# Performance work log

Hardware: AMD Instinct MI355X
Metric: run time of the kernel (lower is better)

The kernel has to match this reference:

```python
import jax, jax.numpy as jnp
import numpy as np

LN2 = float(np.log(2.0))
N_ATOMS = 100_000
N_PAIRS = 2_000_000
F = 64     # number_of_atom_features
R = 16     # number_of_radial_basis_functions
N_RES = 3


def setup_inputs() -> dict:
    key = jax.random.key(0)
    ks = jax.random.split(key, 16)
    s = 0.05
    inp = {
        "pair_indices": jax.random.randint(ks[0], (2, N_PAIRS), 0, N_ATOMS, dtype=jnp.int32),
        "f_ij": jax.random.normal(ks[1], (N_PAIRS, 1, R), dtype=jnp.float32),
        "d_ij": jax.random.uniform(ks[2], (N_PAIRS, 1), dtype=jnp.float32),
        "atomic_embedding": jax.random.normal(ks[3], (N_ATOMS, F), dtype=jnp.float32),
        # AttentionMask parameter G: [F, R]
        "G": jax.random.normal(ks[4], (F, R), dtype=jnp.float32),
        # interaction_i / interaction_j linear layers (stored as [in, out])
        "Wi": jax.random.normal(ks[5], (F, F), dtype=jnp.float32) * s,
        "bi": jnp.zeros((F,), dtype=jnp.float32),
        "Wj": jax.random.normal(ks[6], (F, F), dtype=jnp.float32) * s,
        "bj": jnp.zeros((F,), dtype=jnp.float32),
        # residual blocks, stacked over N_RES
        "res_W1": jax.random.normal(ks[7], (N_RES, F, F), dtype=jnp.float32) * s,
        "res_b1": jnp.zeros((N_RES, F), dtype=jnp.float32),
        "res_W2": jax.random.normal(ks[8], (N_RES, F, F), dtype=jnp.float32) * s,
        "res_b2": jnp.zeros((N_RES, F), dtype=jnp.float32),
        # process_v linear
        "Wv": jax.random.normal(ks[9], (F, F), dtype=jnp.float32) * s,
        "bv": jnp.zeros((F,), dtype=jnp.float32),
    }
    return inp


def reference(pair_indices, f_ij, d_ij, atomic_embedding,
              G, Wi, bi, Wj, bj, res_W1, res_b1, res_W2, res_b2, Wv, bv):
    idx_i, idx_j = pair_indices[0], pair_indices[1]
    f = f_ij.squeeze(1)                                  # [P, R]

    # ShiftedSoftplus on node embeddings
    x = jax.nn.softplus(atomic_embedding) - LN2          # [N, F]

    x_i_prime = jax.nn.softplus(x @ Wi + bi)             # [N, F]
    x_j_prime = jax.nn.softplus(x[idx_j] @ Wj + bj)      # [P, F] (gather)
    f_prime = f @ G.T                                    # [P, F] attention mask

    msg = x_j_prime * f_prime                            # [P, F]
    summed = jax.ops.segment_sum(msg, idx_i, num_segments=atomic_embedding.shape[0])

    v = x_i_prime + summed                               # [N, F]
    for l in range(res_W1.shape[0]):
        h = jax.nn.softplus(v @ res_W1[l] + res_b1[l])
        v = v + (h @ res_W2[l] + res_b2[l])
    return jax.nn.softplus(v) @ Wv + bv
```

## Files before the change

### kernel.cpp

```cpp
#include <hip/hip_runtime.h>
#include <math.h>

#define FDIM 64
#define RDIM 16
#define LN2F 0.69314718055994530942f
#define LTS 68
#define NBINR 14336
#define NCHUNK 64

typedef __bf16 bf8_t __attribute__((ext_vector_type(8)));
typedef float  f4_t  __attribute__((ext_vector_type(4)));
typedef _Float16 h2_t __attribute__((ext_vector_type(2)));

__device__ __forceinline__ float sp(float x) {
    return fmaxf(x, 0.0f) + __logf(1.0f + __expf(-fabsf(x)));
}

__device__ __forceinline__ float fdot2f(h2_t a, h2_t b, float c) {
#if __has_builtin(__builtin_amdgcn_fdot2)
    return __builtin_amdgcn_fdot2(a, b, c, false);
#else
    return c + (float)a[0] * (float)b[0] + (float)a[1] * (float)b[1];
#endif
}

__device__ __forceinline__ void cvt_store16(_Float16* dst, float4 A, float4 B,
                                            float4 C4, float4 D)
{
    h2_t hv[8];
    hv[0] = h2_t{(_Float16)A.x,  (_Float16)A.y};
    hv[1] = h2_t{(_Float16)A.z,  (_Float16)A.w};
    hv[2] = h2_t{(_Float16)B.x,  (_Float16)B.y};
    hv[3] = h2_t{(_Float16)B.z,  (_Float16)B.w};
    hv[4] = h2_t{(_Float16)C4.x, (_Float16)C4.y};
    hv[5] = h2_t{(_Float16)C4.z, (_Float16)C4.w};
    hv[6] = h2_t{(_Float16)D.x,  (_Float16)D.y};
    hv[7] = h2_t{(_Float16)D.z,  (_Float16)D.w};
    *(uint4*)dst       = *(const uint4*)&hv[0];
    *(uint4*)(dst + 8) = *(const uint4*)&hv[4];
}

__global__ __launch_bounds__(256) void k_prep(
    const float* s0, const float* s1, const float* s2, const float* s3,
    const float* s4, const float* s5, const float* s6, const float* s7,
    const float* s8, __bf16* __restrict__ dst)
{
    const float* srcs[9] = {s0, s1, s2, s3, s4, s5, s6, s7, s8};
    const float* W = srcs[blockIdx.x];
    __bf16* d = dst + (size_t)blockIdx.x * 4096;
    for (int slot = threadIdx.x; slot < 512; slot += 256) {
        int f = slot >> 6, l = slot & 63;
        int kt = f >> 2, nt = f & 3;
        int row0 = kt * 32 + (l >> 4) * 8;
        int col = nt * 16 + (l & 15);
#pragma unroll
        for (int j = 0; j < 8; ++j)
            d[slot * 8 + j] = (__bf16)W[(row0 + j) * FDIM + col];
    }
}

__global__ __launch_bounds__(256) void k_hist2(
    const int* __restrict__ idx_i, int* __restrict__ Cmat,
    int P, int N, int nRange)
{
    __shared__ int h[NBINR];
    const int chunk = blockIdx.x / nRange;
    const int range = blockIdx.x % nRange;
    const int lo = range * NBINR;
    const int nb = min(NBINR, N - lo);
    for (int u = threadIdx.x; u < NBINR; u += 256) h[u] = 0;
    __syncthreads();

    const int chunkSz = (P + NCHUNK - 1) / NCHUNK;
    const int cs = chunk * chunkSz;
    const int ce = min(P, cs + chunkSz);
    int p = cs + threadIdx.x;
    for (; p + 768 < ce; p += 1024) {
        int i0 = idx_i[p];
        int i1 = idx_i[p + 256];
        int i2 = idx_i[p + 512];
        int i3 = idx_i[p + 768];
        unsigned u0 = (unsigned)(i0 - lo);
        unsigned u1 = (unsigned)(i1 - lo);
        unsigned u2 = (unsigned)(i2 - lo);
        unsigned u3 = (unsigned)(i3 - lo);
        if (u0 < (unsigned)nb) atomicAdd(&h[u0], 1);
        if (u1 < (unsigned)nb) atomicAdd(&h[u1], 1);
        if (u2 < (unsigned)nb) atomicAdd(&h[u2], 1);
        if (u3 < (unsigned)nb) atomicAdd(&h[u3], 1);
    }
    for (; p < ce; p += 256) {
        unsigned u = (unsigned)(idx_i[p] - lo);
        if (u < (unsigned)nb) atomicAdd(&h[u], 1);
    }
    __syncthreads();
    for (int u = threadIdx.x; u < nb; u += 256)
        Cmat[(size_t)chunk * N + lo + u] = h[u];
}

__global__ __launch_bounds__(256) void k_scanR(
    int* __restrict__ Cmat, int* __restrict__ tot, int N)
{
    const int bA = blockIdx.x * 512 + threadIdx.x;
    const int bB = bA + 256;
    const bool okA = bA < N, okB = bB < N;
    int runA = 0, runB = 0;
    for (int c = 0; c < NCHUNK; ++c) {
        const size_t base = (size_t)c * N;
        if (okA) { int val = Cmat[base + bA]; Cmat[base + bA] = runA; runA += val; }
        if (okB) { int val = Cmat[base + bB]; Cmat[base + bB] = runB; runB += val; }
    }
    if (okA) tot[bA] = runA;
    if (okB) tot[bB] = runB;
}

__device__ __forceinline__ void tile_in(float* T, const float* __restrict__ src,
                                        int a0, int rows, int lane)
{
#pragma unroll 4
    for (int i = 0; i < 16; ++i) {
        int r = i * 4 + (lane >> 4);
        int col = (lane & 15) * 4;
        float4 val = make_float4(0.f, 0.f, 0.f, 0.f);
        if (r < rows) val = *(const float4*)&src[(size_t)(a0 + r) * FDIM + col];
        *(float4*)&T[r * LTS + col] = val;
    }
}

__device__ __forceinline__ void build_a(const float* T, int lane, bool actLn2,
                                        bf8_t (&aF)[4][2])
{
    const int l15 = lane & 15, quad = lane >> 4;
#pragma unroll
    for (int mt = 0; mt < 4; ++mt) {
#pragma unroll
        for (int kt = 0; kt < 2; ++kt) {
            const float* rp = &T[(mt * 16 + l15) * LTS + kt * 32 + quad * 8];
            float4 u0 = *(const float4*)rp;
            float4 u1 = *(const float4*)(rp + 4);
            float e[8] = {u0.x, u0.y, u0.z, u0.w, u1.x, u1.y, u1.z, u1.w};
            bf8_t f;
#pragma unroll
            for (int j = 0; j < 8; ++j) {
                float t = actLn2 ? (sp(e[j]) - LN2F) : e[j];
                f[j] = (__bf16)t;
            }
            aF[mt][kt] = f;
        }
    }
}

__global__ __launch_bounds__(256) void k_atoms(
    const float* __restrict__ emb, const __bf16* __restrict__ wf,
    const float* __restrict__ bi, const float* __restrict__ bj,
    float* __restrict__ v, float* __restrict__ y, int N)
{
    __shared__ float tile[4][64 * LTS];
    const int lane = threadIdx.x & 63;
    const int wv = threadIdx.x >> 6;
    float* T = tile[wv];
    const int l15 = lane & 15, quad = lane >> 4;

    const bf8_t* wiF = (const bf8_t*)wf;
    const bf8_t* wjF = (const bf8_t*)(wf + 4096);
    bf8_t wi[2][4], wj[2][4];
#pragma unroll
    for (int kt = 0; kt < 2; ++kt)
#pragma unroll
        for (int nt = 0; nt < 4; ++nt) {
            wi[kt][nt] = wiF[(kt * 4 + nt) * 64 + lane];
            wj[kt][nt] = wjF[(kt * 4 + nt) * 64 + lane];
        }
    float biv[4], bjv[4];
#pragma unroll
    for (int nt = 0; nt < 4; ++nt) {
        biv[nt] = bi[nt * 16 + l15];
        bjv[nt] = bj[nt * 16 + l15];
    }

    const int nTiles = (N + 63) >> 6;
    for (int t = blockIdx.x * 4 + wv; t < nTiles; t += gridDim.x * 4) {
        const int a0 = t << 6;
        const int rows = min(64, N - a0);
        tile_in(T, emb, a0, rows, lane);
        bf8_t aF[4][2];
        build_a(T, lane, true, aF);
#pragma unroll
        for (int mt = 0; mt < 4; ++mt)
#pragma unroll
            for (int nt = 0; nt < 4; ++nt) {
                f4_t acc = {biv[nt], biv[nt], biv[nt], biv[nt]};
                acc = __builtin_amdgcn_mfma_f32_16x16x32_bf16(aF[mt][0], wi[0][nt], acc, 0, 0, 0);
                acc = __builtin_amdgcn_mfma_f32_16x16x32_bf16(aF[mt][1], wi[1][nt], acc, 0, 0, 0);
#pragma unroll
                for (int reg = 0; reg < 4; ++reg) {
                    int r = mt * 16 + quad * 4 + reg;
                    if (r < rows) v[(size_t)(a0 + r) * FDIM + nt * 16 + l15] = sp(acc[reg]);
                }
            }
#pragma unroll
        for (int mt = 0; mt < 4; ++mt)
#pragma unroll
            for (int nt = 0; nt < 4; ++nt) {
                f4_t acc = {bjv[nt], bjv[nt], bjv[nt], bjv[nt]};
                acc = __builtin_amdgcn_mfma_f32_16x16x32_bf16(aF[mt][0], wj[0][nt], acc, 0, 0, 0);
                acc = __builtin_amdgcn_mfma_f32_16x16x32_bf16(aF[mt][1], wj[1][nt], acc, 0, 0, 0);
#pragma unroll
                for (int reg = 0; reg < 4; ++reg) {
                    int r = mt * 16 + quad * 4 + reg;
                    if (r < rows) y[(size_t)(a0 + r) * FDIM + nt * 16 + l15] = sp(acc[reg]);
                }
            }
    }
}

__global__ __launch_bounds__(256) void k_post(
    const __bf16* __restrict__ wf,
    const float* __restrict__ rb1, const float* __restrict__ rb2,
    const float* __restrict__ bv,
    float* __restrict__ v, int N)
{
    __shared__ float tile[4][64 * LTS];
    const int lane = threadIdx.x & 63;
    const int wv = threadIdx.x >> 6;
    float* T = tile[wv];
    const int l15 = lane & 15, quad = lane >> 4;

    float b1v[3][4], b2v[3][4], bvv[4];
#pragma unroll
    for (int l = 0; l < 3; ++l)
#pragma unroll
        for (int nt = 0; nt < 4; ++nt) {
            b1v[l][nt] = rb1[l * FDIM + nt * 16 + l15];
            b2v[l][nt] = rb2[l * FDIM + nt * 16 + l15];
        }
#pragma unroll
    for (int nt = 0; nt < 4; ++nt) bvv[nt] = bv[nt * 16 + l15];

    const int nTiles = (N + 63) >> 6;
    for (int t = blockIdx.x * 4 + wv; t < nTiles; t += gridDim.x * 4) {
        const int a0 = t << 6;
        const int rows = min(64, N - a0);
        tile_in(T, v, a0, rows, lane);
        float vC[16][4];
#pragma unroll
        for (int mt = 0; mt < 4; ++mt)
#pragma unroll
            for (int nt = 0; nt < 4; ++nt)
#pragma unroll
                for (int reg = 0; reg < 4; ++reg)
                    vC[mt * 4 + nt][reg] =
                        T[(mt * 16 + quad * 4 + reg) * LTS + nt * 16 + l15];

        for (int l = 0; l < 3; ++l) {
            const bf8_t* w1f = (const bf8_t*)(wf + (size_t)(2 * l) * 4096);
            const bf8_t* w2f = (const bf8_t*)(wf + (size_t)(2 * l + 1) * 4096);
            bf8_t aF[4][2];
            build_a(T, lane, false, aF);
#pragma unroll
            for (int mt = 0; mt < 4; ++mt)
#pragma unroll
                for (int nt = 0; nt < 4; ++nt) {
                    f4_t acc = {b1v[l][nt], b1v[l][nt], b1v[l][nt], b1v[l][nt]};
                    acc = __builtin_amdgcn_mfma_f32_16x16x32_bf16(aF[mt][0], w1f[(0 * 4 + nt) * 64 + lane], acc, 0, 0, 0);
                    acc = __builtin_amdgcn_mfma_f32_16x16x32_bf16(aF[mt][1], w1f[(1 * 4 + nt) * 64 + lane], acc, 0, 0, 0);
#pragma unroll
                    for (int reg = 0; reg < 4; ++reg)
                        T[(mt * 16 + quad * 4 + reg) * LTS + nt * 16 + l15] = sp(acc[reg]);
                }
            bf8_t hF[4][2];
            build_a(T, lane, false, hF);
#pragma unroll
            for (int mt = 0; mt < 4; ++mt)
#pragma unroll
                for (int nt = 0; nt < 4; ++nt) {
                    f4_t acc = {b2v[l][nt], b2v[l][nt], b2v[l][nt], b2v[l][nt]};
                    acc = __builtin_amdgcn_mfma_f32_16x16x32_bf16(hF[mt][0], w2f[(0 * 4 + nt) * 64 + lane], acc, 0, 0, 0);
                    acc = __builtin_amdgcn_mfma_f32_16x16x32_bf16(hF[mt][1], w2f[(1 * 4 + nt) * 64 + lane], acc, 0, 0, 0);
#pragma unroll
                    for (int reg = 0; reg < 4; ++reg)
                        vC[mt * 4 + nt][reg] += acc[reg];
                }
            if (l < 2) {
#pragma unroll
                for (int mt = 0; mt < 4; ++mt)
#pragma unroll
                    for (int nt = 0; nt < 4; ++nt)
#pragma unroll
                        for (int reg = 0; reg < 4; ++reg)
                            T[(mt * 16 + quad * 4 + reg) * LTS + nt * 16 + l15] =
                                vC[mt * 4 + nt][reg];
            }
        }
#pragma unroll
        for (int mt = 0; mt < 4; ++mt)
#pragma unroll
            for (int nt = 0; nt < 4; ++nt)
#pragma unroll
                for (int reg = 0; reg < 4; ++reg)
                    T[(mt * 16 + quad * 4 + reg) * LTS + nt * 16 + l15] =
                        sp(vC[mt * 4 + nt][reg]);
        bf8_t fF[4][2];
        build_a(T, lane, false, fF);
        const bf8_t* wvf = (const bf8_t*)(wf + (size_t)6 * 4096);
#pragma unroll
        for (int mt = 0; mt < 4; ++mt)
#pragma unroll
            for (int nt = 0; nt < 4; ++nt) {
                f4_t acc = {bvv[nt], bvv[nt], bvv[nt], bvv[nt]};
                acc = __builtin_amdgcn_mfma_f32_16x16x32_bf16(fF[mt][0], wvf[(0 * 4 + nt) * 64 + lane], acc, 0, 0, 0);
                acc = __builtin_amdgcn_mfma_f32_16x16x32_bf16(fF[mt][1], wvf[(1 * 4 + nt) * 64 + lane], acc, 0, 0, 0);
#pragma unroll
                for (int reg = 0; reg < 4; ++reg) {
                    int r = mt * 16 + quad * 4 + reg;
                    if (r < rows) v[(size_t)(a0 + r) * FDIM + nt * 16 + l15] = acc[reg];
                }
            }
    }
}

__global__ __launch_bounds__(256) void k_scan_a(
    const int* __restrict__ cnt, int* __restrict__ part, int N)
{
    __shared__ int red[256];
    int b = blockIdx.x, t = threadIdx.x;
    int base = b * 1024 + t * 4;
    int s = 0;
#pragma unroll
    for (int i = 0; i < 4; ++i) { int a = base + i; if (a < N) s += cnt[a]; }
    red[t] = s; __syncthreads();
    for (int off = 128; off > 0; off >>= 1) {
        if (t < off) red[t] += red[t + off];
        __syncthreads();
    }
    if (t == 0) part[b] = red[0];
}

__global__ __launch_bounds__(256) void k_scan_b(int* __restrict__ part, int nPart)
{
    __shared__ int lds[256];
    int t = threadIdx.x;
    int base = t * 4;
    int v[4]; int s = 0;
#pragma unroll
    for (int i = 0; i < 4; ++i) { v[i] = (base + i < nPart) ? part[base + i] : 0; s += v[i]; }
    lds[t] = s; __syncthreads();
    int run = s;
    for (int off = 1; off < 256; off <<= 1) {
        int x = (t >= off) ? lds[t - off] : 0;
        __syncthreads();
        lds[t] += x;
        __syncthreads();
    }
    int excl = lds[t] - run;
#pragma unroll
    for (int i = 0; i < 4; ++i) { if (base + i < nPart) { part[base + i] = excl; excl += v[i]; } }
}

__global__ __launch_bounds__(256) void k_scan_c(
    const int* __restrict__ cnt, const int* __restrict__ part,
    int* __restrict__ start, int N, int P)
{
    __shared__ int lds[256];
    int b = blockIdx.x, t = threadIdx.x;
    int base = b * 1024 + t * 4;
    int v[4]; int s = 0;
#pragma unroll
    for (int i = 0; i < 4; ++i) { int a = base + i; v[i] = (a < N) ? cnt[a] : 0; s += v[i]; }
    lds[t] = s; __syncthreads();
    int run = s;
    for (int off = 1; off < 256; off <<= 1) {
        int x = (t >= off) ? lds[t - off] : 0;
        __syncthreads();
        lds[t] += x;
        __syncthreads();
    }
    int pre = part[b] + (lds[t] - run);
#pragma unroll
    for (int i = 0; i < 4; ++i) {
        int a = base + i;
        if (a < N) { start[a] = pre; pre += v[i]; }
    }
    if (b == 0 && t == 0) start[N] = P;
}

__global__ __launch_bounds__(256) void k_scatter2(
    const int* __restrict__ pidx, const int* __restrict__ Cmat,
    const int* __restrict__ start, int2* __restrict__ sorted,
    int P, int N, int nRange)
{
    __shared__ int cur[NBINR];
    const int chunk = blockIdx.x / nRange;
    const int range = blockIdx.x % nRange;
    const int lo = range * NBINR;
    const int nb = min(NBINR, N - lo);
    for (int u = threadIdx.x; u < nb; u += 256)
        cur[u] = start[lo + u] + Cmat[(size_t)chunk * N + lo + u];
    __syncthreads();

    const int chunkSz = (P + NCHUNK - 1) / NCHUNK;
    const int cs = chunk * chunkSz;
    const int ce = min(P, cs + chunkSz);
    int p = cs + threadIdx.x;
    for (; p + 768 < ce; p += 1024) {
        int i0 = pidx[p];
        int i1 = pidx[p + 256];
        int i2 = pidx[p + 512];
        int i3 = pidx[p + 768];
        int j0 = pidx[P + p];
        int j1 = pidx[P + p + 256];
        int j2 = pidx[P + p + 512];
        int j3 = pidx[P + p + 768];
        unsigned u0 = (unsigned)(i0 - lo);
        unsigned u1 = (unsigned)(i1 - lo);
        unsigned u2 = (unsigned)(i2 - lo);
        unsigned u3 = (unsigned)(i3 - lo);
        if (u0 < (unsigned)nb) { int pos = atomicAdd(&cur[u0], 1); sorted[pos] = make_int2(p, j0); }
        if (u1 < (unsigned)nb) { int pos = atomicAdd(&cur[u1], 1); sorted[pos] = make_int2(p + 256, j1); }
        if (u2 < (unsigned)nb) { int pos = atomicAdd(&cur[u2], 1); sorted[pos] = make_int2(p + 512, j2); }
        if (u3 < (unsigned)nb) { int pos = atomicAdd(&cur[u3], 1); sorted[pos] = make_int2(p + 768, j3); }
    }
    for (; p < ce; p += 256) {
        int i = pidx[p];
        unsigned u = (unsigned)(i - lo);
        if (u < (unsigned)nb) {
            int j = pidx[P + p];
            int pos = atomicAdd(&cur[u], 1);
            sorted[pos] = make_int2(p, j);
        }
    }
}

__global__ __launch_bounds__(256) void k_gatherF(
    const int2* __restrict__ sorted, const float* __restrict__ f_ij,
    int* __restrict__ sortedJ, _Float16* __restrict__ sortedF, int P)
{
    int t = blockIdx.x * blockDim.x + threadIdx.x;
    int n = gridDim.x * blockDim.x;
    int pos = t;
    for (; pos + 3 * n < P; pos += 4 * n) {
        int2 E0 = sorted[pos];
        int2 E1 = sorted[pos + n];
        int2 E2 = sorted[pos + 2 * n];
        int2 E3 = sorted[pos + 3 * n];
        const float4* f0 = (const float4*)(f_ij + (size_t)E0.x * RDIM);
        const float4* f1 = (const float4*)(f_ij + (size_t)E1.x * RDIM);
        const float4* f2 = (const float4*)(f_ij + (size_t)E2.x * RDIM);
        const float4* f3 = (const float4*)(f_ij + (size_t)E3.x * RDIM);
        float4 a0 = f0[0], b0 = f0[1], c0 = f0[2], d0 = f0[3];
        float4 a1 = f1[0], b1 = f1[1], c1 = f1[2], d1 = f1[3];
        float4 a2 = f2[0], b2 = f2[1], c2 = f2[2], d2 = f2[3];
        float4 a3 = f3[0], b3 = f3[1], c3 = f3[2], d3 = f3[3];
        sortedJ[pos]         = E0.y;
        sortedJ[pos + n]     = E1.y;
        sortedJ[pos + 2 * n] = E2.y;
        sortedJ[pos + 3 * n] = E3.y;
        cvt_store16(sortedF + (size_t)pos * 16,           a0, b0, c0, d0);
        cvt_store16(sortedF + (size_t)(pos + n) * 16,     a1, b1, c1, d1);
        cvt_store16(sortedF + (size_t)(pos + 2 * n) * 16, a2, b2, c2, d2);
        cvt_store16(sortedF + (size_t)(pos + 3 * n) * 16, a3, b3, c3, d3);
    }
    for (; pos < P; pos += n) {
        int2 E = sorted[pos];
        const float4* fp = (const float4*)(f_ij + (size_t)E.x * RDIM);
        float4 A = fp[0], B = fp[1], C4 = fp[2], D = fp[3];
        sortedJ[pos] = E.y;
        cvt_store16(sortedF + (size_t)pos * 16, A, B, C4, D);
    }
}

__global__ __launch_bounds__(256) void k_seg(
    const int* __restrict__ sortedJ, const _Float16* __restrict__ sortedF,
    const int* __restrict__ start, const float* __restrict__ G,
    const float* __restrict__ y, float* __restrict__ v, int N)
{
    const int c = threadIdx.x & 63;
    const int w = __builtin_amdgcn_readfirstlane((blockIdx.x << 2) | (threadIdx.x >> 6));
    const int nw = gridDim.x << 2;

    h2_t g2[8];
    {
        const float4* gp = (const float4*)(G + c * RDIM);
        float4 g0 = gp[0], g1 = gp[1], g2v = gp[2], g3 = gp[3];
        g2[0] = h2_t{(_Float16)g0.x, (_Float16)g0.y};
        g2[1] = h2_t{(_Float16)g0.z, (_Float16)g0.w};
        g2[2] = h2_t{(_Float16)g1.x, (_Float16)g1.y};
        g2[3] = h2_t{(_Float16)g1.z, (_Float16)g1.w};
        g2[4] = h2_t{(_Float16)g2v.x, (_Float16)g2v.y};
        g2[5] = h2_t{(_Float16)g2v.z, (_Float16)g2v.w};
        g2[6] = h2_t{(_Float16)g3.x, (_Float16)g3.y};
        g2[7] = h2_t{(_Float16)g3.z, (_Float16)g3.w};
    }

    for (int a = w; a < N; a += nw) {
        const int s = __builtin_amdgcn_readfirstlane(start[a]);
        const int e = __builtin_amdgcn_readfirstlane(start[a + 1]);
        float vold = v[(size_t)a * FDIM + c];
        float acc0 = 0.f, acc1 = 0.f, acc2 = 0.f, acc3 = 0.f;

        for (int base = s; base < e; base += 64) {
            const int nn = (e - base < 64) ? (e - base) : 64;
            const int li = (c < nn) ? c : (nn - 1);
            const int jkv = sortedJ[base + li];

            int k = 0;
            for (; k + 8 <= nn; k += 8) {
                int jj[8];
#pragma unroll
                for (int u = 0; u < 8; ++u)
                    jj[u] = __builtin_amdgcn_readlane(jkv, k + u);
                float yv[8];
#pragma unroll
                for (int u = 0; u < 8; ++u)
                    yv[u] = y[(size_t)jj[u] * FDIM + c];
                const h2_t* f2 = (const h2_t*)(sortedF + (size_t)(base + k) * 16);
#pragma unroll
                for (int u = 0; u < 8; ++u) {
                    float d = 0.f;
#pragma unroll
                    for (int r = 0; r < 8; ++r)
                        d = fdot2f(f2[u * 8 + r], g2[r], d);
                    if ((u & 3) == 0) acc0 = fmaf(d, yv[u], acc0);
                    else if ((u & 3) == 1) acc1 = fmaf(d, yv[u], acc1);
                    else if ((u & 3) == 2) acc2 = fmaf(d, yv[u], acc2);
                    else acc3 = fmaf(d, yv[u], acc3);
                }
            }
            for (; k < nn; ++k) {
                const int j0 = __builtin_amdgcn_readlane(jkv, k);
                float y0 = y[(size_t)j0 * FDIM + c];
                const h2_t* f2 = (const h2_t*)(sortedF + (size_t)(base + k) * 16);
                float d = 0.f;
#pragma unroll
                for (int r = 0; r < 8; ++r)
                    d = fdot2f(f2[r], g2[r], d);
                acc0 = fmaf(d, y0, acc0);
            }
        }

        v[(size_t)a * FDIM + c] = vold + (acc0 + acc1) + (acc2 + acc3);
    }
}

extern "C" void kernel_launch(void* const* d_in, const int* in_sizes, int n_in,
                              void* d_out, int out_size, void* d_ws, size_t ws_size,
                              hipStream_t stream)
{
    const int*   pidx = (const int*)d_in[0];
    const float* f_ij = (const float*)d_in[1];
    const float* emb  = (const float*)d_in[3];
    const float* G    = (const float*)d_in[4];
    const float* Wi   = (const float*)d_in[5];
    const float* bi   = (const float*)d_in[6];
    const float* Wj   = (const float*)d_in[7];
    const float* bj   = (const float*)d_in[8];
    const float* rW1  = (const float*)d_in[9];
    const float* rb1  = (const float*)d_in[10];
    const float* rW2  = (const float*)d_in[11];
    const float* rb2  = (const float*)d_in[12];
    const float* Wv   = (const float*)d_in[13];
    const float* bv   = (const float*)d_in[14];

    const int P = in_sizes[0] / 2;
    const int N = in_sizes[3] / FDIM;

    float* v = (float*)d_out;

    char* ws = (char*)d_ws;
    size_t off = 0;
    float*  y      = (float*)(ws + off);
    int*    Cmat   = (int*)(ws + off);    off += (size_t)N * FDIM * 4;
    int*    tot    = (int*)(ws + off);    off += (size_t)N * 4;
    int*    start  = (int*)(ws + off);    off += (size_t)(N + 1) * 4;
    off = (off + 15) & ~(size_t)15;
    int*    part   = (int*)(ws + off);    off += (size_t)4096 * 4;
    off = (off + 15) & ~(size_t)15;
    int2*   sorted = (int2*)(ws + off);   off += (size_t)P * 8;
    off = (off + 15) & ~(size_t)15;
    int*    sortedJ = (int*)(ws + off);   off += (size_t)P * 4;
    off = (off + 63) & ~(size_t)63;
    _Float16* sortedF = (_Float16*)(ws + off); off += (size_t)P * 16 * 2;
    off = (off + 15) & ~(size_t)15;
    __bf16* wf     = (__bf16*)(ws + off); off += (size_t)9 * 4096 * 2;

    const int nRange = (N + NBINR - 1) / NBINR;
    const int nPart = (N + 1023) / 1024;
    const int nTiles = (N + 63) >> 6;
    const int gTiles = (nTiles + 3) / 4;

    dim3 blk(256);
    k_prep<<<9, blk, 0, stream>>>(Wi, Wj, rW1, rW2, rW1 + 4096, rW2 + 4096,
                                  rW1 + 8192, rW2 + 8192, Wv, wf);
    k_hist2<<<NCHUNK * nRange, blk, 0, stream>>>(pidx, Cmat, P, N, nRange);
    k_scanR<<<(N + 511) / 512, blk, 0, stream>>>(Cmat, tot, N);
    k_scan_a<<<nPart, blk, 0, stream>>>(tot, part, N);
    k_scan_b<<<1, blk, 0, stream>>>(part, nPart);
    k_scan_c<<<nPart, blk, 0, stream>>>(tot, part, start, N, P);
    k_scatter2<<<NCHUNK * nRange, blk, 0, stream>>>(pidx, Cmat, start, sorted, P, N, nRange);
    k_gatherF<<<2048, blk, 0, stream>>>(sorted, f_ij, sortedJ, sortedF, P);
    k_atoms<<<gTiles, blk, 0, stream>>>(emb, wf, bi, bj, v, y, N);
    k_seg<<<4096, blk, 0, stream>>>(sortedJ, sortedF, start, G, y, v, N);
    k_post<<<gTiles, blk, 0, stream>>>(wf + (size_t)2 * 4096, rb1, rb2, bv, v, N);
}
```

Baseline: 635.6 us.

## Store y as fp16 and scatter f_ij via inverse permutation instead of gather

```diff
diff --git a/kernel.cpp b/kernel.cpp
--- a/kernel.cpp
+++ b/kernel.cpp
@@ -153,7 +153,7 @@
 __global__ __launch_bounds__(256) void k_atoms(
     const float* __restrict__ emb, const __bf16* __restrict__ wf,
     const float* __restrict__ bi, const float* __restrict__ bj,
-    float* __restrict__ v, float* __restrict__ y, int N)
+    float* __restrict__ v, _Float16* __restrict__ y16, int N)
 {
     __shared__ float tile[4][64 * LTS];
     const int lane = threadIdx.x & 63;
@@ -208,7 +208,8 @@
 #pragma unroll
                 for (int reg = 0; reg < 4; ++reg) {
                     int r = mt * 16 + quad * 4 + reg;
-                    if (r < rows) y[(size_t)(a0 + r) * FDIM + nt * 16 + l15] = sp(acc[reg]);
+                    if (r < rows)
+                        y16[(size_t)(a0 + r) * FDIM + nt * 16 + l15] = (_Float16)sp(acc[reg]);
                 }
             }
     }
@@ -386,8 +387,8 @@
 
 __global__ __launch_bounds__(256) void k_scatter2(
     const int* __restrict__ pidx, const int* __restrict__ Cmat,
-    const int* __restrict__ start, int2* __restrict__ sorted,
-    int P, int N, int nRange)
+    const int* __restrict__ start, int* __restrict__ sortedJ,
+    int* __restrict__ invPos, int P, int N, int nRange)
 {
     __shared__ int cur[NBINR];
     const int chunk = blockIdx.x / nRange;
@@ -415,10 +416,10 @@
         unsigned u1 = (unsigned)(i1 - lo);
         unsigned u2 = (unsigned)(i2 - lo);
         unsigned u3 = (unsigned)(i3 - lo);
-        if (u0 < (unsigned)nb) { int pos = atomicAdd(&cur[u0], 1); sorted[pos] = make_int2(p, j0); }
-        if (u1 < (unsigned)nb) { int pos = atomicAdd(&cur[u1], 1); sorted[pos] = make_int2(p + 256, j1); }
-        if (u2 < (unsigned)nb) { int pos = atomicAdd(&cur[u2], 1); sorted[pos] = make_int2(p + 512, j2); }
-        if (u3 < (unsigned)nb) { int pos = atomicAdd(&cur[u3], 1); sorted[pos] = make_int2(p + 768, j3); }
+        if (u0 < (unsigned)nb) { int pos = atomicAdd(&cur[u0], 1); sortedJ[pos] = j0; invPos[p] = pos; }
+        if (u1 < (unsigned)nb) { int pos = atomicAdd(&cur[u1], 1); sortedJ[pos] = j1; invPos[p + 256] = pos; }
+        if (u2 < (unsigned)nb) { int pos = atomicAdd(&cur[u2], 1); sortedJ[pos] = j2; invPos[p + 512] = pos; }
+        if (u3 < (unsigned)nb) { int pos = atomicAdd(&cur[u3], 1); sortedJ[pos] = j3; invPos[p + 768] = pos; }
     }
     for (; p < ce; p += 256) {
         int i = pidx[p];
@@ -426,53 +427,49 @@
         if (u < (unsigned)nb) {
             int j = pidx[P + p];
             int pos = atomicAdd(&cur[u], 1);
-            sorted[pos] = make_int2(p, j);
+            sortedJ[pos] = j;
+            invPos[p] = pos;
         }
     }
 }
 
-__global__ __launch_bounds__(256) void k_gatherF(
-    const int2* __restrict__ sorted, const float* __restrict__ f_ij,
-    int* __restrict__ sortedJ, _Float16* __restrict__ sortedF, int P)
+__global__ __launch_bounds__(256) void k_gatherF2(
+    const float* __restrict__ f_ij, const int* __restrict__ invPos,
+    _Float16* __restrict__ sortedF, int P)
 {
     int t = blockIdx.x * blockDim.x + threadIdx.x;
     int n = gridDim.x * blockDim.x;
-    int pos = t;
-    for (; pos + 3 * n < P; pos += 4 * n) {
-        int2 E0 = sorted[pos];
-        int2 E1 = sorted[pos + n];
-        int2 E2 = sorted[pos + 2 * n];
-        int2 E3 = sorted[pos + 3 * n];
-        const float4* f0 = (const float4*)(f_ij + (size_t)E0.x * RDIM);
-        const float4* f1 = (const float4*)(f_ij + (size_t)E1.x * RDIM);
-        const float4* f2 = (const float4*)(f_ij + (size_t)E2.x * RDIM);
-        const float4* f3 = (const float4*)(f_ij + (size_t)E3.x * RDIM);
+    int p = t;
+    for (; p + 3 * n < P; p += 4 * n) {
+        int q0 = invPos[p];
+        int q1 = invPos[p + n];
+        int q2 = invPos[p + 2 * n];
+        int q3 = invPos[p + 3 * n];
+        const float4* f0 = (const float4*)(f_ij + (size_t)p * RDIM);
+        const float4* f1 = (const float4*)(f_ij + (size_t)(p + n) * RDIM);
+        const float4* f2 = (const float4*)(f_ij + (size_t)(p + 2 * n) * RDIM);
+        const float4* f3 = (const float4*)(f_ij + (size_t)(p + 3 * n) * RDIM);
         float4 a0 = f0[0], b0 = f0[1], c0 = f0[2], d0 = f0[3];
         float4 a1 = f1[0], b1 = f1[1], c1 = f1[2], d1 = f1[3];
         float4 a2 = f2[0], b2 = f2[1], c2 = f2[2], d2 = f2[3];
         float4 a3 = f3[0], b3 = f3[1], c3 = f3[2], d3 = f3[3];
-        sortedJ[pos]         = E0.y;
-        sortedJ[pos + n]     = E1.y;
-        sortedJ[pos + 2 * n] = E2.y;
-        sortedJ[pos + 3 * n] = E3.y;
-        cvt_store16(sortedF + (size_t)pos * 16,           a0, b0, c0, d0);
-        cvt_store16(sortedF + (size_t)(pos + n) * 16,     a1, b1, c1, d1);
-        cvt_store16(sortedF + (size_t)(pos + 2 * n) * 16, a2, b2, c2, d2);
-        cvt_store16(sortedF + (size_t)(pos + 3 * n) * 16, a3, b3, c3, d3);
-    }
-    for (; pos < P; pos += n) {
-        int2 E = sorted[pos];
-        const float4* fp = (const float4*)(f_ij + (size_t)E.x * RDIM);
+        cvt_store16(sortedF + (size_t)q0 * 16, a0, b0, c0, d0);
+        cvt_store16(sortedF + (size_t)q1 * 16, a1, b1, c1, d1);
+        cvt_store16(sortedF + (size_t)q2 * 16, a2, b2, c2, d2);
+        cvt_store16(sortedF + (size_t)q3 * 16, a3, b3, c3, d3);
+    }
+    for (; p < P; p += n) {
+        int q = invPos[p];
+        const float4* fp = (const float4*)(f_ij + (size_t)p * RDIM);
         float4 A = fp[0], B = fp[1], C4 = fp[2], D = fp[3];
-        sortedJ[pos] = E.y;
-        cvt_store16(sortedF + (size_t)pos * 16, A, B, C4, D);
+        cvt_store16(sortedF + (size_t)q * 16, A, B, C4, D);
     }
 }
 
 __global__ __launch_bounds__(256) void k_seg(
     const int* __restrict__ sortedJ, const _Float16* __restrict__ sortedF,
     const int* __restrict__ start, const float* __restrict__ G,
-    const float* __restrict__ y, float* __restrict__ v, int N)
+    const _Float16* __restrict__ y16, float* __restrict__ v, int N)
 {
     const int c = threadIdx.x & 63;
     const int w = __builtin_amdgcn_readfirstlane((blockIdx.x << 2) | (threadIdx.x >> 6));
@@ -512,7 +509,7 @@
                 float yv[8];
 #pragma unroll
                 for (int u = 0; u < 8; ++u)
-                    yv[u] = y[(size_t)jj[u] * FDIM + c];
+                    yv[u] = (float)y16[(size_t)jj[u] * FDIM + c];
                 const h2_t* f2 = (const h2_t*)(sortedF + (size_t)(base + k) * 16);
 #pragma unroll
                 for (int u = 0; u < 8; ++u) {
@@ -528,7 +525,7 @@
             }
             for (; k < nn; ++k) {
                 const int j0 = __builtin_amdgcn_readlane(jkv, k);
-                float y0 = y[(size_t)j0 * FDIM + c];
+                float y0 = (float)y16[(size_t)j0 * FDIM + c];
                 const h2_t* f2 = (const h2_t*)(sortedF + (size_t)(base + k) * 16);
                 float d = 0.f;
 #pragma unroll
@@ -568,16 +565,16 @@
 
     char* ws = (char*)d_ws;
     size_t off = 0;
-    float*  y      = (float*)(ws + off);
+    _Float16* y16  = (_Float16*)(ws + off);
     int*    Cmat   = (int*)(ws + off);    off += (size_t)N * FDIM * 4;
     int*    tot    = (int*)(ws + off);    off += (size_t)N * 4;
     int*    start  = (int*)(ws + off);    off += (size_t)(N + 1) * 4;
     off = (off + 15) & ~(size_t)15;
     int*    part   = (int*)(ws + off);    off += (size_t)4096 * 4;
     off = (off + 15) & ~(size_t)15;
-    int2*   sorted = (int2*)(ws + off);   off += (size_t)P * 8;
+    int*    sortedJ = (int*)(ws + off);   off += (size_t)P * 4;
     off = (off + 15) & ~(size_t)15;
-    int*    sortedJ = (int*)(ws + off);   off += (size_t)P * 4;
+    int*    invPos  = (int*)(ws + off);   off += (size_t)P * 4;
     off = (off + 63) & ~(size_t)63;
     _Float16* sortedF = (_Float16*)(ws + off); off += (size_t)P * 16 * 2;
     off = (off + 15) & ~(size_t)15;
@@ -596,9 +593,10 @@
     k_scan_a<<<nPart, blk, 0, stream>>>(tot, part, N);
     k_scan_b<<<1, blk, 0, stream>>>(part, nPart);
     k_scan_c<<<nPart, blk, 0, stream>>>(tot, part, start, N, P);
-    k_scatter2<<<NCHUNK * nRange, blk, 0, stream>>>(pidx, Cmat, start, sorted, P, N, nRange);
-    k_gatherF<<<2048, blk, 0, stream>>>(sorted, f_ij, sortedJ, sortedF, P);
-    k_atoms<<<gTiles, blk, 0, stream>>>(emb, wf, bi, bj, v, y, N);
-    k_seg<<<4096, blk, 0, stream>>>(sortedJ, sortedF, start, G, y, v, N);
+    k_scatter2<<<NCHUNK * nRange, blk, 0, stream>>>(pidx, Cmat, start, sortedJ,
+                                                    invPos, P, N, nRange);
+    k_gatherF2<<<2048, blk, 0, stream>>>(f_ij, invPos, sortedF, P);
+    k_atoms<<<gTiles, blk, 0, stream>>>(emb, wf, bi, bj, v, y16, N);
+    k_seg<<<4096, blk, 0, stream>>>(sortedJ, sortedF, start, G, y16, v, N);
     k_post<<<gTiles, blk, 0, stream>>>(wf + (size_t)2 * 4096, rb1, rb2, bv, v, N);
 }
```

Result: no change. 640.6 us (+0.8%).
